# Optimization experiments

Hardware: AMD Instinct MI355X
Metric: run time of the kernel (lower is better)

The kernel has to match this reference:

```python
import jax, jax.numpy as jnp
import numpy as np

C_IN_LSTM = 46
HIDDEN = 16
SEQ_LEN = 512      # == c_in of value_embedding
D_MODEL = 512
BATCH = 1024


def setup_inputs() -> dict:
    key = jax.random.key(0)
    ks = jax.random.split(key, 12)
    s = 1.0 / np.sqrt(HIDDEN)
    inp = {
        "x": jax.random.normal(ks[0], (BATCH, SEQ_LEN, C_IN_LSTM), jnp.float32),
        "x_mark": jax.random.normal(ks[1], (BATCH, SEQ_LEN, 4), jnp.float32),
        # LSTM params (torch layout: [4*H, in], gate order i,f,g,o)
        "W_ih": jax.random.uniform(ks[2], (4 * HIDDEN, C_IN_LSTM), jnp.float32, -s, s),
        "W_hh": jax.random.uniform(ks[3], (4 * HIDDEN, HIDDEN), jnp.float32, -s, s),
        "b_ih": jax.random.uniform(ks[4], (4 * HIDDEN,), jnp.float32, -s, s),
        "b_hh": jax.random.uniform(ks[5], (4 * HIDDEN,), jnp.float32, -s, s),
        # fc: Linear(16, 46)
        "fc_W": jax.random.uniform(ks[6], (C_IN_LSTM, HIDDEN), jnp.float32, -s, s),
        "fc_b": jax.random.uniform(ks[7], (C_IN_LSTM,), jnp.float32, -s, s),
        # value_embedding: Linear(c_in=T, d_model)
        "ve_W": jax.random.normal(ks[8], (D_MODEL, SEQ_LEN), jnp.float32) * (1.0 / np.sqrt(SEQ_LEN)),
        "ve_b": jnp.zeros((D_MODEL,), jnp.float32),
    }
    return inp


def _lstm(x, W_ih, W_hh, b_ih, b_hh):
    # x: [B, T, C]. Precompute input projection for all steps (one big GEMM).
    B = x.shape[0]
    x_proj = jnp.einsum("btc,gc->btg", x, W_ih) + (b_ih + b_hh)  # [B, T, 4H]
    x_proj = jnp.swapaxes(x_proj, 0, 1)  # [T, B, 4H]

    def step(carry, gx):
        h, c = carry
        gates = gx + h @ W_hh.T  # [B, 4H]
        i, f, g, o = jnp.split(gates, 4, axis=-1)
        i = jax.nn.sigmoid(i)
        f = jax.nn.sigmoid(f)
        g = jnp.tanh(g)
        o = jax.nn.sigmoid(o)
        c = f * c + i * g
        h = o * jnp.tanh(c)
        return (h, c), h

    h0 = jnp.zeros((B, HIDDEN), x.dtype)
    c0 = jnp.zeros((B, HIDDEN), x.dtype)
    _, hs = jax.lax.scan(step, (h0, c0), x_proj)  # hs: [T, B, H]
    return jnp.swapaxes(hs, 0, 1)  # [B, T, H]


def reference(x, x_mark, W_ih, W_hh, b_ih, b_hh, fc_W, fc_b, ve_W, ve_b):
    # x_mark is accepted but unused (matches original forward).
    h = _lstm(x, W_ih, W_hh, b_ih, b_hh)              # [B, T, 16]
    y = h @ fc_W.T + fc_b                             # [B, T, 46] (squeeze(-1) is a no-op)
    y = jnp.swapaxes(y, 1, 2)                         # [B, 46, T]
    out = y @ ve_W.T + ve_b                           # [B, 46, d_model]
    # dropout is identity in eval mode
    return out
```

## Files before the change

### kernel.cpp

```cpp
#include <hip/hip_runtime.h>


typedef unsigned short u16;
typedef unsigned int u32;
typedef float v4f __attribute__((ext_vector_type(4)));
typedef __bf16 v8bf __attribute__((ext_vector_type(8)));

#define LOG2E 1.44269504088896340736f

#define BATCH 1024
#define TSEQ 512
#define CIN 46
#define NH 16
#define NCH 46
#define DM 512

static constexpr size_t XP_BYTES  = (size_t)BATCH * TSEQ * 64 * 2;
static constexpr size_t HSF_BYTES = (size_t)BATCH * 16 * 512 * 2;
static constexpr size_t VEF_BYTES = (size_t)32 * 16 * 512 * 2;

static __device__ __forceinline__ u16 f2bf(float f) {
  u32 u = __float_as_uint(f);
  u32 r = (u + 0x7FFFu + ((u >> 16) & 1u)) >> 16;
  return (u16)r;
}
static __device__ __forceinline__ float bf2f(u16 h) {
  return __uint_as_float(((u32)h) << 16);
}
static __device__ __forceinline__ u32 cvt_pk_bf16(float lo, float hi) {
  u32 r;
  asm("v_cvt_pk_bf16_f32 %0, %1, %2" : "=v"(r) : "v"(lo), "v"(hi));
  return r;
}

template <int K>
static __device__ __forceinline__ float qb(float x) {
  return __int_as_float(__builtin_amdgcn_mov_dpp(__float_as_int(x), K * 0x55, 0xF, 0xF, true));
}

__global__ void k_vefrag(const float* __restrict__ veW, u16* __restrict__ vef) {
  int D0 = blockIdx.x >> 4, T0 = blockIdx.x & 15;
  int lane = threadIdx.x;
  int d = D0 * 16 + (lane & 15);
  int t = T0 * 32 + (lane >> 4) * 8;
  const float* src = veW + (size_t)d * 512 + t;
  float4 v0 = *(const float4*)(src);
  float4 v1 = *(const float4*)(src + 4);
  uint4 o;
  o.x = cvt_pk_bf16(v0.x, v0.y);
  o.y = cvt_pk_bf16(v0.z, v0.w);
  o.z = cvt_pk_bf16(v1.x, v1.y);
  o.w = cvt_pk_bf16(v1.z, v1.w);
  *(uint4*)(vef + ((size_t)(D0 * 16 + T0)) * 512 + lane * 8) = o;
}

__global__ void k_vesum(const float* __restrict__ veW, float* __restrict__ S) {
  int t = blockIdx.x * 256 + threadIdx.x;
  int d = t >> 4, seg = t & 15;
  const float4* r = (const float4*)(veW + (size_t)d * 512 + seg * 32);
  float a0 = 0.f, a1 = 0.f, a2 = 0.f, a3 = 0.f;
#pragma unroll
  for (int i = 0; i < 8; ++i) {
    float4 v = r[i];
    a0 += v.x; a1 += v.y; a2 += v.z; a3 += v.w;
  }
  float s = (a0 + a1) + (a2 + a3);
#pragma unroll
  for (int o = 1; o < 16; o <<= 1) s += __shfl_xor(s, o, 64);
  if (seg == 0) S[d] = s;
}

__global__ __launch_bounds__(256) void k_xprojm(
    const float* __restrict__ x, const float* __restrict__ Wih,
    const float* __restrict__ bih, const float* __restrict__ bhh,
    u16* __restrict__ xp) {
  int lane = threadIdx.x & 63;
  int warp = threadIdx.x >> 6;
  int l15 = lane & 15, lg = lane >> 4;
  long wid = (long)blockIdx.x * 4 + warp;
  long rowbase = wid * 32;

  v8bf bfr[4][2];
#pragma unroll
  for (int q = 0; q < 4; ++q) {
    int g = q * 16 + l15;
#pragma unroll
    for (int ks = 0; ks < 2; ++ks) {
      int koff = ks * 32 + lg * 8;
      float bv[8];
#pragma unroll
      for (int e = 0; e < 8; ++e) {
        int c = koff + e;
        int cc = c < 45 ? c : 45;
        float v = Wih[g * 46 + cc];
        bv[e] = (c < 46) ? v : 0.f;
      }
      uint4 wp;
      wp.x = cvt_pk_bf16(bv[0], bv[1]);
      wp.y = cvt_pk_bf16(bv[2], bv[3]);
      wp.z = cvt_pk_bf16(bv[4], bv[5]);
      wp.w = cvt_pk_bf16(bv[6], bv[7]);
      bfr[q][ks] = __builtin_bit_cast(v8bf, wp);
    }
  }

  v4f acc[2][4];
#pragma unroll
  for (int q = 0; q < 4; ++q) {
    float bb = bih[q * 16 + l15] + bhh[q * 16 + l15];
#pragma unroll
    for (int mt = 0; mt < 2; ++mt) acc[mt][q] = (v4f){bb, bb, bb, bb};
  }

#pragma unroll
  for (int mt = 0; mt < 2; ++mt) {
    long row = rowbase + mt * 16 + l15;
    const float* xb = x + row * 46;
#pragma unroll
    for (int ks = 0; ks < 2; ++ks) {
      int koff = ks * 32 + lg * 8;
      float av[8];
#pragma unroll
      for (int i = 0; i < 4; ++i) {
        int c0 = koff + 2 * i;
        int cc = c0 < 44 ? c0 : 44;
        float2 v2 = *(const float2*)(xb + cc);
        av[2 * i] = v2.x;
        av[2 * i + 1] = v2.y;
      }
      if (ks == 1) {
#pragma unroll
        for (int e = 0; e < 8; ++e)
          if (koff + e >= 46) av[e] = 0.f;
      }
      uint4 ap;
      ap.x = cvt_pk_bf16(av[0], av[1]);
      ap.y = cvt_pk_bf16(av[2], av[3]);
      ap.z = cvt_pk_bf16(av[4], av[5]);
      ap.w = cvt_pk_bf16(av[6], av[7]);
      v8bf a = __builtin_bit_cast(v8bf, ap);
#pragma unroll
      for (int q = 0; q < 4; ++q)
        acc[mt][q] = __builtin_amdgcn_mfma_f32_16x16x32_bf16(a, bfr[q][ks], acc[mt][q], 0, 0, 0);
    }
  }

#pragma unroll
  for (int mt = 0; mt < 2; ++mt) {
    long rowblk = wid * 2 + mt;
#pragma unroll
    for (int q = 0; q < 4; ++q) {
      uint2 o;
      o.x = cvt_pk_bf16(acc[mt][q][0], acc[mt][q][1]);
      o.y = cvt_pk_bf16(acc[mt][q][2], acc[mt][q][3]);
      *(uint2*)(xp + ((rowblk * 4 + q) * 256 + lane * 4)) = o;
    }
  }
}

__global__ __launch_bounds__(256) void k_lstm(
    const u16* __restrict__ xp, const float* __restrict__ Whh,
    u16* __restrict__ hsf) {
  int lane = threadIdx.x & 63;
  int warp = __builtin_amdgcn_readfirstlane((int)(threadIdx.x >> 6));
  int b = blockIdx.x * 4 + warp;
  int q = lane & 3, j = lane >> 2;
  int rowt = q * 16 + j;
  float w[NH];
#pragma unroll
  for (int k = 0; k < NH; ++k) w[k] = Whh[rowt * NH + k];
  float kmul = (q == 2) ? (-2.f * LOG2E) : (-LOG2E);
  float ka = (q == 2) ? 2.f : 1.f;
  float kb = (q == 2) ? -1.f : 0.f;
  float c = 0.f;
  float hreg[NH];
#pragma unroll
  for (int k = 0; k < NH; ++k) hreg[k] = 0.f;

  __shared__ __align__(16) u16 stage[4][512];
  u16* st = stage[warp];

  const u16* xq = xp + (size_t)b * 32768;
  u16* hb = hsf + (size_t)b * 16 * 512;

  uint2 bufA[8], bufB[8];
  auto LOADC = [&](uint2* buf, int p) {
#pragma unroll
    for (int c2 = 0; c2 < 8; ++c2) {
      int mt = 2 * p + (c2 >> 2), t4 = c2 & 3;
      buf[c2] = *(const uint2*)(xq + ((size_t)(mt * 4 + q) * 256 + (t4 * 16 + j) * 4));
    }
  };
  LOADC(bufA, 0);

  auto GX = [&](uint2* buf, int i) -> float {
    int c2 = ((i >> 4) << 2) | ((i >> 2) & 3);
    u32 word = (i & 2) ? buf[c2].y : buf[c2].x;
    u16 hx = (i & 1) ? (u16)(word >> 16) : (u16)(word & 0xFFFFu);
    return bf2f(hx);
  };

  auto STEP = [&](float gx, int i) {
    float a0 = fmaf(hreg[0], w[0], gx);
    float a1 = hreg[1] * w[1];
    float a2 = hreg[2] * w[2];
    float a3 = hreg[3] * w[3];
#pragma unroll
    for (int k = 4; k < 16; k += 4) {
      a0 = fmaf(hreg[k + 0], w[k + 0], a0);
      a1 = fmaf(hreg[k + 1], w[k + 1], a1);
      a2 = fmaf(hreg[k + 2], w[k + 2], a2);
      a3 = fmaf(hreg[k + 3], w[k + 3], a3);
    }
    float v = (a0 + a1) + (a2 + a3);
    float e = __builtin_amdgcn_exp2f(v * kmul);
    float s = __builtin_amdgcn_rcpf(1.f + e);
    float act = fmaf(s, ka, kb);
    float iv = qb<0>(act), fv = qb<1>(act), gv = qb<2>(act), ov = qb<3>(act);
    c = fmaf(fv, c, iv * gv);
    float e2 = __builtin_amdgcn_exp2f(c * (-2.f * LOG2E));
    float s2 = __builtin_amdgcn_rcpf(1.f + e2);
    float th = fmaf(s2, 2.f, -1.f);
    float hv = ov * th;
    if (q == (i >> 3)) st[(j + 16 * (i >> 3)) * 8 + (i & 7)] = f2bf(hv);
#pragma unroll
    for (int k = 0; k < 16; ++k)
      hreg[k] = __int_as_float(__builtin_amdgcn_readlane(__float_as_int(hv), 4 * k));
  };

  for (int p = 0; p < 16; p += 2) {
    LOADC(bufB, p + 1);
#pragma unroll
    for (int i = 0; i < 32; ++i) STEP(GX(bufA, i), i);
    uint4 dv = *(uint4*)(st + lane * 8);
    *(uint4*)(hb + (size_t)p * 512 + lane * 8) = dv;
    if (p + 2 < 16) LOADC(bufA, p + 2);
#pragma unroll
    for (int i = 0; i < 32; ++i) STEP(GX(bufB, i), i);
    uint4 dv2 = *(uint4*)(st + lane * 8);
    *(uint4*)(hb + (size_t)(p + 1) * 512 + lane * 8) = dv2;
  }
}

__global__ __launch_bounds__(256, 1) void k_gemm(
    const u16* __restrict__ hsf, const u16* __restrict__ vef,
    const float* __restrict__ fcW, const float* __restrict__ fcb,
    const float* __restrict__ S, const float* __restrict__ veb,
    float* __restrict__ out) {
  int lane = threadIdx.x & 63;
  int warp = __builtin_amdgcn_readfirstlane((int)(threadIdx.x >> 6));
  int bbase = blockIdx.x * 4;
  __shared__ __align__(16) float Glds[4][2][16][128];

  v4f acc[4][8];
#pragma unroll
  for (int bi = 0; bi < 4; ++bi)
#pragma unroll
    for (int dt = 0; dt < 8; ++dt) acc[bi][dt] = (v4f){0.f, 0.f, 0.f, 0.f};

  const u16* ap0 = hsf + (size_t)bbase * 16 * 512 + lane * 8;
  const u16* bp0 = vef + (size_t)warp * 8 * 16 * 512 + lane * 8;

#pragma unroll 2
  for (int kk = 0; kk < 16; ++kk) {
    v8bf a[4], bf[8];
#pragma unroll
    for (int bi = 0; bi < 4; ++bi) {
      uint4 t = *(const uint4*)(ap0 + ((size_t)bi * 16 + kk) * 512);
      a[bi] = __builtin_bit_cast(v8bf, t);
    }
#pragma unroll
    for (int dt = 0; dt < 8; ++dt) {
      uint4 t = *(const uint4*)(bp0 + ((size_t)dt * 16 + kk) * 512);
      bf[dt] = __builtin_bit_cast(v8bf, t);
    }
#pragma unroll
    for (int bi = 0; bi < 4; ++bi)
#pragma unroll
      for (int dt = 0; dt < 8; ++dt)
        acc[bi][dt] = __builtin_amdgcn_mfma_f32_16x16x32_bf16(a[bi], bf[dt], acc[bi][dt], 0, 0, 0);
  }

  int m4 = (lane >> 4) * 4;
  int nn = lane & 15;
  int dq = lane & 31;
  int bsel = lane >> 5;
  v4f S4 = *(const v4f*)(S + warp * 128 + dq * 4);
  v4f veb4 = *(const v4f*)(veb + warp * 128 + dq * 4);

#pragma unroll
  for (int hh = 0; hh < 2; ++hh) {
#pragma unroll
    for (int bi2 = 0; bi2 < 2; ++bi2)
#pragma unroll
      for (int dt = 0; dt < 8; ++dt)
#pragma unroll
        for (int r = 0; r < 4; ++r)
          Glds[warp][bi2][m4 + r][dt * 16 + nn] = acc[2 * hh + bi2][dt][r];
    v4f g4[16];
#pragma unroll
    for (int jj = 0; jj < 16; ++jj)
      g4[jj] = *(const v4f*)&Glds[warp][bsel][jj][dq * 4];
    size_t b = (size_t)bbase + 2 * hh + bsel;
    float* ob = out + b * (size_t)(NCH * DM) + warp * 128 + dq * 4;
#pragma unroll 2
    for (int ch = 0; ch < NCH; ++ch) {
      float fb = fcb[ch];
      v4f o4 = S4 * fb + veb4;
#pragma unroll
      for (int jj = 0; jj < 16; ++jj) o4 += fcW[ch * 16 + jj] * g4[jj];
      *(v4f*)(ob + (size_t)ch * DM) = o4;
    }
  }
}

extern "C" void kernel_launch(void* const* d_in, const int* in_sizes, int n_in,
                              void* d_out, int out_size, void* d_ws, size_t ws_size,
                              hipStream_t stream) {
  (void)in_sizes; (void)n_in; (void)out_size; (void)ws_size;
  const float* x   = (const float*)d_in[0];
  const float* Wih = (const float*)d_in[2];
  const float* Whh = (const float*)d_in[3];
  const float* bih = (const float*)d_in[4];
  const float* bhh = (const float*)d_in[5];
  const float* fcW = (const float*)d_in[6];
  const float* fcb = (const float*)d_in[7];
  const float* veW = (const float*)d_in[8];
  const float* veb = (const float*)d_in[9];
  float* out = (float*)d_out;

  char* ws = (char*)d_ws;
  u16* xp   = (u16*)ws;
  u16* hsf  = (u16*)(ws + XP_BYTES);
  u16* vef  = (u16*)(ws + XP_BYTES + HSF_BYTES);
  float* S  = (float*)(ws + XP_BYTES + HSF_BYTES + VEF_BYTES);

  hipLaunchKernelGGL(k_vefrag, dim3(512), dim3(64), 0, stream, veW, vef);
  hipLaunchKernelGGL(k_vesum, dim3(32), dim3(256), 0, stream, veW, S);
  hipLaunchKernelGGL(k_xprojm, dim3(4096), dim3(256), 0, stream, x, Wih, bih, bhh, xp);
  hipLaunchKernelGGL(k_lstm, dim3(256), dim3(256), 0, stream, xp, Whh, hsf);
  hipLaunchKernelGGL(k_gemm, dim3(256), dim3(256), 0, stream, hsf, vef, fcW, fcb, S, veb, out);
}
```

Baseline: 328.1 us.

## Pack LSTM hidden outputs in registers and launch one wave per batch

The LSTM kernel stops staging each step's bf16 hidden value through shared memory with a per-step conditional store. Each lane now keeps the values it owns in registers, packs them with the hardware bf16 convert, and writes one 16-byte vector per chunk straight to global memory. The launch also changes from 256-thread blocks covering four batches to 64-thread blocks covering one batch, so waves are scheduled independently. The cost is extra select instructions on every step and more registers held live per lane.

Measured after the change: 358.1 us. 9.2% more time.

```diff
diff --git a/kernel.cpp b/kernel.cpp
--- a/kernel.cpp
+++ b/kernel.cpp
@@ -19,11 +19,6 @@
 static constexpr size_t HSF_BYTES = (size_t)BATCH * 16 * 512 * 2;
 static constexpr size_t VEF_BYTES = (size_t)32 * 16 * 512 * 2;
 
-static __device__ __forceinline__ u16 f2bf(float f) {
-  u32 u = __float_as_uint(f);
-  u32 r = (u + 0x7FFFu + ((u >> 16) & 1u)) >> 16;
-  return (u16)r;
-}
 static __device__ __forceinline__ float bf2f(u16 h) {
   return __uint_as_float(((u32)h) << 16);
 }
@@ -158,12 +153,11 @@
   }
 }
 
-__global__ __launch_bounds__(256) void k_lstm(
+__global__ __launch_bounds__(64, 1) void k_lstm(
     const u16* __restrict__ xp, const float* __restrict__ Whh,
     u16* __restrict__ hsf) {
   int lane = threadIdx.x & 63;
-  int warp = __builtin_amdgcn_readfirstlane((int)(threadIdx.x >> 6));
-  int b = blockIdx.x * 4 + warp;
+  int b = blockIdx.x;
   int q = lane & 3, j = lane >> 2;
   int rowt = q * 16 + j;
   float w[NH];
@@ -177,9 +171,6 @@
 #pragma unroll
   for (int k = 0; k < NH; ++k) hreg[k] = 0.f;
 
-  __shared__ __align__(16) u16 stage[4][512];
-  u16* st = stage[warp];
-
   const u16* xq = xp + (size_t)b * 32768;
   u16* hb = hsf + (size_t)b * 16 * 512;
 
@@ -200,7 +191,7 @@
     return bf2f(hx);
   };
 
-  auto STEP = [&](float gx, int i) {
+  auto STEP = [&](float gx) -> float {
     float a0 = fmaf(hreg[0], w[0], gx);
     float a1 = hreg[1] * w[1];
     float a2 = hreg[2] * w[2];
@@ -222,23 +213,35 @@
     float s2 = __builtin_amdgcn_rcpf(1.f + e2);
     float th = fmaf(s2, 2.f, -1.f);
     float hv = ov * th;
-    if (q == (i >> 3)) st[(j + 16 * (i >> 3)) * 8 + (i & 7)] = f2bf(hv);
 #pragma unroll
     for (int k = 0; k < 16; ++k)
       hreg[k] = __int_as_float(__builtin_amdgcn_readlane(__float_as_int(hv), 4 * k));
+    return hv;
+  };
+
+  auto CHUNK = [&](uint2* buf, int p) {
+    uint4 d = {0u, 0u, 0u, 0u};
+    float sv = 0.f;
+#pragma unroll
+    for (int g = 0; g < 4; ++g) {
+      bool cap = (q == g);
+      float h0 = STEP(GX(buf, 8 * g + 0)); sv = cap ? h0 : sv;
+      float h1 = STEP(GX(buf, 8 * g + 1)); { u32 pk = cvt_pk_bf16(sv, h1); d.x = cap ? pk : d.x; }
+      float h2 = STEP(GX(buf, 8 * g + 2)); sv = cap ? h2 : sv;
+      float h3 = STEP(GX(buf, 8 * g + 3)); { u32 pk = cvt_pk_bf16(sv, h3); d.y = cap ? pk : d.y; }
+      float h4 = STEP(GX(buf, 8 * g + 4)); sv = cap ? h4 : sv;
+      float h5 = STEP(GX(buf, 8 * g + 5)); { u32 pk = cvt_pk_bf16(sv, h5); d.z = cap ? pk : d.z; }
+      float h6 = STEP(GX(buf, 8 * g + 6)); sv = cap ? h6 : sv;
+      float h7 = STEP(GX(buf, 8 * g + 7)); { u32 pk = cvt_pk_bf16(sv, h7); d.w = cap ? pk : d.w; }
+    }
+    *(uint4*)(hb + (size_t)p * 512 + (j + 16 * q) * 8) = d;
   };
 
   for (int p = 0; p < 16; p += 2) {
     LOADC(bufB, p + 1);
-#pragma unroll
-    for (int i = 0; i < 32; ++i) STEP(GX(bufA, i), i);
-    uint4 dv = *(uint4*)(st + lane * 8);
-    *(uint4*)(hb + (size_t)p * 512 + lane * 8) = dv;
+    CHUNK(bufA, p);
     if (p + 2 < 16) LOADC(bufA, p + 2);
-#pragma unroll
-    for (int i = 0; i < 32; ++i) STEP(GX(bufB, i), i);
-    uint4 dv2 = *(uint4*)(st + lane * 8);
-    *(uint4*)(hb + (size_t)(p + 1) * 512 + lane * 8) = dv2;
+    CHUNK(bufB, p + 1);
   }
 }
 
@@ -338,6 +341,6 @@
   hipLaunchKernelGGL(k_vefrag, dim3(512), dim3(64), 0, stream, veW, vef);
   hipLaunchKernelGGL(k_vesum, dim3(32), dim3(256), 0, stream, veW, S);
   hipLaunchKernelGGL(k_xprojm, dim3(4096), dim3(256), 0, stream, x, Wih, bih, bhh, xp);
-  hipLaunchKernelGGL(k_lstm, dim3(256), dim3(256), 0, stream, xp, Whh, hsf);
+  hipLaunchKernelGGL(k_lstm, dim3(1024), dim3(64), 0, stream, xp, Whh, hsf);
   hipLaunchKernelGGL(k_gemm, dim3(256), dim3(256), 0, stream, hsf, vef, fcW, fcb, S, veb, out);
 }
```
